# Kernel optimization log

Hardware: AMD Instinct MI355X
Metric: run time of the kernel (lower is better)

## Reference

```python
import jax, jax.numpy as jnp
import numpy as np

N = 50000      # total nodes
C = 128        # in_channels
G = 4          # num_groups
B = 50         # number of graphs
NPG = N // B   # nodes per graph = 1000
E = 250000     # total edges (intra-graph)
COUT = 128     # conv out_channels


def setup_inputs() -> dict:
    key = jax.random.key(0)
    ks = jax.random.split(key, 6)
    sc = 1.0 / np.sqrt(C)
    x = jax.random.normal(ks[0], (N, C), dtype=jnp.float32)
    W_group = jax.random.normal(ks[1], (C, G), dtype=jnp.float32) * sc
    W_self = jax.random.normal(ks[2], (C, COUT), dtype=jnp.float32) * sc
    W_nbr = jax.random.normal(ks[3], (C, COUT), dtype=jnp.float32) * sc
    b = jnp.zeros((COUT,), dtype=jnp.float32)
    # intra-graph edges: E//B edges per graph, endpoints offset by graph id
    epg = E // B
    offs = (jnp.arange(E, dtype=jnp.int32) // epg) * NPG
    src = offs + jax.random.randint(ks[4], (E,), 0, NPG, dtype=jnp.int32)
    dst = offs + jax.random.randint(ks[5], (E,), 0, NPG, dtype=jnp.int32)
    edge_index = jnp.stack([src, dst])
    batch = (jnp.arange(N, dtype=jnp.int32) // NPG)
    # expanded node e = i*G*NPG + g*NPG + j maps back to original node i*NPG + j
    eidx = jnp.arange(G * N, dtype=jnp.int32)
    group_ptr = (eidx // (G * NPG)) * NPG + (eidx % NPG)
    return dict(x=x, W_group=W_group, W_self=W_self, W_nbr=W_nbr, b=b,
                edge_index=edge_index, batch=batch, group_ptr=group_ptr)


def reference(x, W_group, W_self, W_nbr, b, edge_index, batch, group_ptr):
    # soft group assignment: s = softmax(x @ W_group).T -> [G, N]
    s = jax.nn.softmax(x @ W_group, axis=-1).T
    # outer-product expansion: [G, N, C]
    ex = s[:, :, None] * x[None, :, :]
    # per-graph cat ordering: (g, graph i, local j) -> i*G*NPG + g*NPG + j
    ex = ex.reshape(G, B, NPG, C).transpose(1, 0, 2, 3).reshape(G * N, C)
    # expanded adjacency: replicate each graph's edges once per group
    src, dst = edge_index[0], edge_index[1]
    goff = jnp.arange(G, dtype=src.dtype)[:, None] * NPG            # [G, 1]
    src_exp = ((src // NPG) * (G * NPG))[None, :] + goff + (src % NPG)[None, :]
    dst_exp = ((dst // NPG) * (G * NPG))[None, :] + goff + (dst % NPG)[None, :]
    src_exp = src_exp.reshape(-1)
    dst_exp = dst_exp.reshape(-1)
    # GraphConv on expanded graph: self transform + sum-aggregated neighbor transform
    msg = (ex @ W_nbr)[src_exp]                                      # [G*E, COUT]
    agg = jax.ops.segment_sum(msg, dst_exp, num_segments=G * N)
    out = ex @ W_self + agg + b                                      # [G*N, COUT]
    # scatter-reduce G group copies back onto N original nodes
    return jax.ops.segment_sum(out, group_ptr, num_segments=N)
```

## Files before the change

### kernel.cpp

```cpp
#include <hip/hip_runtime.h>

constexpr int N_NODES  = 50000;
constexpr int C_IN     = 128;
constexpr int C_OUT    = 128;
constexpr int E_EDGES  = 250000;
constexpr int G_GRP    = 4;
constexpr int NXCD     = 8;
constexpr int CAP      = 32;
constexpr int CAP1     = 8;
constexpr int TMF      = 64;


typedef __attribute__((ext_vector_type(8))) short     short8;
typedef __attribute__((ext_vector_type(4))) float     f32x4;
typedef __attribute__((ext_vector_type(2))) unsigned  u32x2;

__device__ __forceinline__ unsigned short f2bf(float f) {
    unsigned u = __builtin_bit_cast(unsigned, f);
    u += 0x7fffu + ((u >> 16) & 1u);
    return (unsigned short)(u >> 16);
}
__device__ __forceinline__ unsigned pack2(float lo, float hi) {
    return (unsigned)f2bf(lo) | ((unsigned)f2bf(hi) << 16);
}
__device__ __forceinline__ int xcd_swizzle(int bid, int nblocks) {
    int q = nblocks / NXCD, r = nblocks % NXCD;
    int xcd = bid % NXCD, lid = bid / NXCD;
    return (xcd < r ? xcd * (q + 1) : r * (q + 1) + (xcd - r) * q) + lid;
}

constexpr int BKT_I4   = N_NODES * CAP / 4;
constexpr int BKT_BLKS = (BKT_I4 + 255) / 256;
constexpr int CNT_BLKS = (N_NODES / 4 + 255) / 256;
constexpr int WT_BLKS  = (C_OUT * 256) / 256;

__global__ __launch_bounds__(256) void zero_prep_kernel(
    int* __restrict__ cnt, int* __restrict__ buckets,
    const float* __restrict__ Wself, const float* __restrict__ Wnbr,
    unsigned short* __restrict__ WT)
{
    int b = blockIdx.x;
    if (b < BKT_BLKS) {
        int idx = b * 256 + threadIdx.x;
        if (idx < BKT_I4) {
            int n = idx >> 3;
            reinterpret_cast<int4*>(buckets)[idx] = make_int4(n, n, n, n);
        }
    } else if (b < BKT_BLKS + CNT_BLKS) {
        int idx = (b - BKT_BLKS) * 256 + threadIdx.x;
        if (idx < N_NODES / 4)
            reinterpret_cast<int4*>(cnt)[idx] = make_int4(0, 0, 0, 0);
    } else {
        int idx = (b - BKT_BLKS - CNT_BLKS) * 256 + threadIdx.x;
        int c = idx >> 8, k = idx & 255;
        float v = (k < 128) ? Wself[k * C_OUT + c] : Wnbr[(k - 128) * C_OUT + c];
        WT[idx] = f2bf(v);
    }
}

constexpr int EDGE_BLOCKS = (E_EDGES + 255) / 256;

__global__ __launch_bounds__(256) void fill_kernel(
    const int* __restrict__ src, const int* __restrict__ dst,
    int* __restrict__ cnt, int* __restrict__ buckets)
{
    int e = blockIdx.x * 256 + threadIdx.x;
    if (e < E_EDGES) {
        int d = dst[e];
        int pos = atomicAdd(&cnt[d], 1);
        if (pos < CAP) buckets[(size_t)d * CAP + pos] = src[e];
    }
}

constexpr int FUSED_BLOCKS = (N_NODES + TMF - 1) / TMF;

__global__ __launch_bounds__(512, 2) void fused_kernel(
    const float* __restrict__ x,
    const int* __restrict__ cnt,
    const int* __restrict__ buckets,
    const unsigned short* __restrict__ WT,
    const float* __restrict__ bias,
    float* __restrict__ out)
{
    __shared__ unsigned char Ab[TMF * 512];

    int wg = xcd_swizzle(blockIdx.x, FUSED_BLOCKS);
    const int tid  = threadIdx.x;
    const int row0 = wg * TMF;

    #pragma unroll
    for (int i = 0; i < 4; ++i) {
        int idx = tid + i * 512;
        int r = idx >> 5, q = idx & 31;
        int n = row0 + r;
        float4 v = make_float4(0.f, 0.f, 0.f, 0.f);
        if (n < N_NODES) v = reinterpret_cast<const float4*>(x)[(size_t)n * 32 + q];
        int byte = (r * 512 + q * 8) ^ ((r & 7) << 4);
        *reinterpret_cast<u32x2*>(&Ab[byte]) = u32x2{pack2(v.x, v.y), pack2(v.z, v.w)};
    }

    {
        const int slot = tid >> 5;
        const int q    = tid & 31;
        const float4* x4 = reinterpret_cast<const float4*>(x);
        #pragma unroll
        for (int h = 0; h < 4; ++h) {
            int r  = slot + h * 16;
            int n  = row0 + r;
            int nc = (n < N_NODES) ? n : (N_NODES - 1);
            int d  = cnt[nc];
            if (d > CAP) d = CAP;
            if (n >= N_NODES) d = 0;
            const int4* sp4 = reinterpret_cast<const int4*>(buckets + (size_t)nc * CAP);

            float ax = 0.f, ay = 0.f, az = 0.f, aw = 0.f;
            {
                int4 sA = sp4[0], sB = sp4[1];
                int sl[8] = {sA.x, sA.y, sA.z, sA.w, sB.x, sB.y, sB.z, sB.w};
                #pragma unroll
                for (int k = 0; k < 8; ++k) {
                    float4 v = x4[(size_t)sl[k] * 32 + q];
                    if (k < d) { ax += v.x; ay += v.y; az += v.z; aw += v.w; }
                }
            }
            if (d > CAP1) {
                #pragma unroll
                for (int t = 0; t < 3; ++t) {
                    int4 sC = sp4[2 + 2 * t], sD = sp4[3 + 2 * t];
                    int sl[8] = {sC.x, sC.y, sC.z, sC.w, sD.x, sD.y, sD.z, sD.w};
                    #pragma unroll
                    for (int k = 0; k < 8; ++k) {
                        float4 v = x4[(size_t)sl[k] * 32 + q];
                        if (8 + t * 8 + k < d) { ax += v.x; ay += v.y; az += v.z; aw += v.w; }
                    }
                }
            }
            int byte = (r * 512 + 256 + q * 8) ^ ((r & 7) << 4);
            *reinterpret_cast<u32x2*>(&Ab[byte]) = u32x2{pack2(ax, ay), pack2(az, aw)};
        }
    }
    __syncthreads();

    const int lane = tid & 63;
    const int w    = tid >> 6;
    const int rt   = w >> 1;
    const int ct0  = (w & 1) * 4;

    short8 a[8];
    {
        int r  = rt * 16 + (lane & 15);
        int kb = (lane >> 4) * 16;
        #pragma unroll
        for (int ks = 0; ks < 8; ++ks) {
            int byte = (r * 512 + ks * 64 + kb) ^ ((r & 7) << 4);
            a[ks] = *reinterpret_cast<const short8*>(&Ab[byte]);
        }
    }

    #pragma unroll
    for (int cti = 0; cti < 4; ++cti) {
        int c = (ct0 + cti) * 16 + (lane & 15);
        const short8* bp = reinterpret_cast<const short8*>(WT + (size_t)c * 256)
                           + (lane >> 4);
        f32x4 acc = {0.f, 0.f, 0.f, 0.f};
        #pragma unroll
        for (int ks = 0; ks < 8; ++ks)
            acc = __builtin_amdgcn_mfma_f32_16x16x32_bf16(a[ks], bp[ks * 4],
                                                          acc, 0, 0, 0);
        float bv = (float)G_GRP * bias[c];
        #pragma unroll
        for (int ii = 0; ii < 4; ++ii) {
            int rr = row0 + rt * 16 + (lane >> 4) * 4 + ii;
            if (rr < N_NODES) out[(size_t)rr * C_OUT + c] = acc[ii] + bv;
        }
    }
}

extern "C" void kernel_launch(void* const* d_in, const int* in_sizes, int n_in,
                              void* d_out, int out_size, void* d_ws, size_t ws_size,
                              hipStream_t stream)
{
    const float* x     = (const float*)d_in[0];
    const float* Wself = (const float*)d_in[2];
    const float* Wnbr  = (const float*)d_in[3];
    const float* bias  = (const float*)d_in[4];
    const int*   eidx  = (const int*)d_in[5];

    const int* src = eidx;
    const int* dst = eidx + E_EDGES;

    int* cnt     = (int*)d_ws;
    int* buckets = cnt + N_NODES;
    unsigned short* WT = (unsigned short*)(buckets + (size_t)N_NODES * CAP);

    float* out = (float*)d_out;

    zero_prep_kernel<<<BKT_BLKS + CNT_BLKS + WT_BLKS, 256, 0, stream>>>(
        cnt, buckets, Wself, Wnbr, WT);

    fill_kernel<<<EDGE_BLOCKS, 256, 0, stream>>>(src, dst, cnt, buckets);

    fused_kernel<<<FUSED_BLOCKS, 512, 0, stream>>>(x, cnt, buckets, WT, bias, out);
}
```

Baseline: 70.25 us.

## Pre-convert x to bf16 for gathers and drop bucket pre-fill

A prep kernel now converts x to a bf16 copy once, and the fused kernel gathers neighbor rows from that copy, which halves the bytes per gather and skips per-use conversion. The bucket pre-fill (writing self indices) is removed; unused slots are masked by clamping their index to 0 and multiplying by a zero mask. The launch-bounds occupancy hint is dropped. This adds an extra full pass over x and sums neighbors from bf16-rounded inputs, which changes precision slightly.

Result: no change. 71.33 us (+1.5%).

```diff
diff --git a/kernel.cpp b/kernel.cpp
--- a/kernel.cpp
+++ b/kernel.cpp
@@ -14,6 +14,7 @@
 typedef __attribute__((ext_vector_type(8))) short     short8;
 typedef __attribute__((ext_vector_type(4))) float     f32x4;
 typedef __attribute__((ext_vector_type(2))) unsigned  u32x2;
+typedef __attribute__((ext_vector_type(4))) unsigned  u32x4;
 
 __device__ __forceinline__ unsigned short f2bf(float f) {
     unsigned u = __builtin_bit_cast(unsigned, f);
@@ -23,38 +24,45 @@
 __device__ __forceinline__ unsigned pack2(float lo, float hi) {
     return (unsigned)f2bf(lo) | ((unsigned)f2bf(hi) << 16);
 }
+__device__ __forceinline__ float bflo(unsigned u) {
+    return __builtin_bit_cast(float, u << 16);
+}
+__device__ __forceinline__ float bfhi(unsigned u) {
+    return __builtin_bit_cast(float, u & 0xffff0000u);
+}
 __device__ __forceinline__ int xcd_swizzle(int bid, int nblocks) {
     int q = nblocks / NXCD, r = nblocks % NXCD;
     int xcd = bid % NXCD, lid = bid / NXCD;
     return (xcd < r ? xcd * (q + 1) : r * (q + 1) + (xcd - r) * q) + lid;
 }
 
-constexpr int BKT_I4   = N_NODES * CAP / 4;
-constexpr int BKT_BLKS = (BKT_I4 + 255) / 256;
 constexpr int CNT_BLKS = (N_NODES / 4 + 255) / 256;
 constexpr int WT_BLKS  = (C_OUT * 256) / 256;
-
-__global__ __launch_bounds__(256) void zero_prep_kernel(
-    int* __restrict__ cnt, int* __restrict__ buckets,
+constexpr int XB_BLKS  = (N_NODES * 16) / 256;
+
+__global__ __launch_bounds__(256) void prep_kernel(
+    int* __restrict__ cnt,
     const float* __restrict__ Wself, const float* __restrict__ Wnbr,
-    unsigned short* __restrict__ WT)
+    unsigned short* __restrict__ WT,
+    const float* __restrict__ x, unsigned short* __restrict__ xb)
 {
     int b = blockIdx.x;
-    if (b < BKT_BLKS) {
+    if (b < CNT_BLKS) {
         int idx = b * 256 + threadIdx.x;
-        if (idx < BKT_I4) {
-            int n = idx >> 3;
-            reinterpret_cast<int4*>(buckets)[idx] = make_int4(n, n, n, n);
-        }
-    } else if (b < BKT_BLKS + CNT_BLKS) {
-        int idx = (b - BKT_BLKS) * 256 + threadIdx.x;
         if (idx < N_NODES / 4)
             reinterpret_cast<int4*>(cnt)[idx] = make_int4(0, 0, 0, 0);
-    } else {
-        int idx = (b - BKT_BLKS - CNT_BLKS) * 256 + threadIdx.x;
+    } else if (b < CNT_BLKS + WT_BLKS) {
+        int idx = (b - CNT_BLKS) * 256 + threadIdx.x;
         int c = idx >> 8, k = idx & 255;
         float v = (k < 128) ? Wself[k * C_OUT + c] : Wnbr[(k - 128) * C_OUT + c];
         WT[idx] = f2bf(v);
+    } else {
+        int idx = (b - CNT_BLKS - WT_BLKS) * 256 + threadIdx.x;
+        const float4* xp = reinterpret_cast<const float4*>(x) + (size_t)idx * 2;
+        float4 v0 = xp[0], v1 = xp[1];
+        u32x4 o{pack2(v0.x, v0.y), pack2(v0.z, v0.w),
+                pack2(v1.x, v1.y), pack2(v1.z, v1.w)};
+        reinterpret_cast<u32x4*>(xb)[idx] = o;
     }
 }
 
@@ -74,8 +82,8 @@
 
 constexpr int FUSED_BLOCKS = (N_NODES + TMF - 1) / TMF;
 
-__global__ __launch_bounds__(512, 2) void fused_kernel(
-    const float* __restrict__ x,
+__global__ __launch_bounds__(512) void fused_kernel(
+    const unsigned short* __restrict__ xb,
     const int* __restrict__ cnt,
     const int* __restrict__ buckets,
     const unsigned short* __restrict__ WT,
@@ -93,16 +101,17 @@
         int idx = tid + i * 512;
         int r = idx >> 5, q = idx & 31;
         int n = row0 + r;
-        float4 v = make_float4(0.f, 0.f, 0.f, 0.f);
-        if (n < N_NODES) v = reinterpret_cast<const float4*>(x)[(size_t)n * 32 + q];
+        u32x2 pk{0u, 0u};
+        if (n < N_NODES)
+            pk = *reinterpret_cast<const u32x2*>(&xb[(size_t)n * 128 + q * 4]);
         int byte = (r * 512 + q * 8) ^ ((r & 7) << 4);
-        *reinterpret_cast<u32x2*>(&Ab[byte]) = u32x2{pack2(v.x, v.y), pack2(v.z, v.w)};
+        *reinterpret_cast<u32x2*>(&Ab[byte]) = pk;
     }
 
     {
         const int slot = tid >> 5;
         const int q    = tid & 31;
-        const float4* x4 = reinterpret_cast<const float4*>(x);
+        const u32x2* xb2 = reinterpret_cast<const u32x2*>(xb);
         #pragma unroll
         for (int h = 0; h < 4; ++h) {
             int r  = slot + h * 16;
@@ -113,30 +122,57 @@
             if (n >= N_NODES) d = 0;
             const int4* sp4 = reinterpret_cast<const int4*>(buckets + (size_t)nc * CAP);
 
-            float ax = 0.f, ay = 0.f, az = 0.f, aw = 0.f;
+            float a0 = 0.f, a1 = 0.f, a2 = 0.f, a3 = 0.f;
             {
                 int4 sA = sp4[0], sB = sp4[1];
-                int sl[8] = {sA.x, sA.y, sA.z, sA.w, sB.x, sB.y, sB.z, sB.w};
-                #pragma unroll
-                for (int k = 0; k < 8; ++k) {
-                    float4 v = x4[(size_t)sl[k] * 32 + q];
-                    if (k < d) { ax += v.x; ay += v.y; az += v.z; aw += v.w; }
-                }
+                int s0 = (0 < d) ? sA.x : 0, s1 = (1 < d) ? sA.y : 0;
+                int s2 = (2 < d) ? sA.z : 0, s3 = (3 < d) ? sA.w : 0;
+                int s4 = (4 < d) ? sB.x : 0, s5 = (5 < d) ? sB.y : 0;
+                int s6 = (6 < d) ? sB.z : 0, s7 = (7 < d) ? sB.w : 0;
+                u32x2 w0 = xb2[(size_t)s0 * 32 + q];
+                u32x2 w1 = xb2[(size_t)s1 * 32 + q];
+                u32x2 w2 = xb2[(size_t)s2 * 32 + q];
+                u32x2 w3 = xb2[(size_t)s3 * 32 + q];
+                u32x2 w4 = xb2[(size_t)s4 * 32 + q];
+                u32x2 w5 = xb2[(size_t)s5 * 32 + q];
+                u32x2 w6 = xb2[(size_t)s6 * 32 + q];
+                u32x2 w7 = xb2[(size_t)s7 * 32 + q];
+                #define ACC(W, K)                                               \
+                    { float m = (K < d) ? 1.f : 0.f;                            \
+                      a0 = fmaf(m, bflo(W.x), a0); a1 = fmaf(m, bfhi(W.x), a1); \
+                      a2 = fmaf(m, bflo(W.y), a2); a3 = fmaf(m, bfhi(W.y), a3); }
+                ACC(w0, 0) ACC(w1, 1) ACC(w2, 2) ACC(w3, 3)
+                ACC(w4, 4) ACC(w5, 5) ACC(w6, 6) ACC(w7, 7)
             }
             if (d > CAP1) {
                 #pragma unroll
                 for (int t = 0; t < 3; ++t) {
                     int4 sC = sp4[2 + 2 * t], sD = sp4[3 + 2 * t];
-                    int sl[8] = {sC.x, sC.y, sC.z, sC.w, sD.x, sD.y, sD.z, sD.w};
-                    #pragma unroll
-                    for (int k = 0; k < 8; ++k) {
-                        float4 v = x4[(size_t)sl[k] * 32 + q];
-                        if (8 + t * 8 + k < d) { ax += v.x; ay += v.y; az += v.z; aw += v.w; }
-                    }
+                    int base = 8 + t * 8;
+                    int s0 = (base + 0 < d) ? sC.x : 0, s1 = (base + 1 < d) ? sC.y : 0;
+                    int s2 = (base + 2 < d) ? sC.z : 0, s3 = (base + 3 < d) ? sC.w : 0;
+                    int s4 = (base + 4 < d) ? sD.x : 0, s5 = (base + 5 < d) ? sD.y : 0;
+                    int s6 = (base + 6 < d) ? sD.z : 0, s7 = (base + 7 < d) ? sD.w : 0;
+                    u32x2 w0 = xb2[(size_t)s0 * 32 + q];
+                    u32x2 w1 = xb2[(size_t)s1 * 32 + q];
+                    u32x2 w2 = xb2[(size_t)s2 * 32 + q];
+                    u32x2 w3 = xb2[(size_t)s3 * 32 + q];
+                    u32x2 w4 = xb2[(size_t)s4 * 32 + q];
+                    u32x2 w5 = xb2[(size_t)s5 * 32 + q];
+                    u32x2 w6 = xb2[(size_t)s6 * 32 + q];
+                    u32x2 w7 = xb2[(size_t)s7 * 32 + q];
+                    #define ACC2(W, K)                                              \
+                        { float m = (base + K < d) ? 1.f : 0.f;                     \
+                          a0 = fmaf(m, bflo(W.x), a0); a1 = fmaf(m, bfhi(W.x), a1); \
+                          a2 = fmaf(m, bflo(W.y), a2); a3 = fmaf(m, bfhi(W.y), a3); }
+                    ACC2(w0, 0) ACC2(w1, 1) ACC2(w2, 2) ACC2(w3, 3)
+                    ACC2(w4, 4) ACC2(w5, 5) ACC2(w6, 6) ACC2(w7, 7)
+                    #undef ACC2
                 }
             }
+            #undef ACC
             int byte = (r * 512 + 256 + q * 8) ^ ((r & 7) << 4);
-            *reinterpret_cast<u32x2*>(&Ab[byte]) = u32x2{pack2(ax, ay), pack2(az, aw)};
+            *reinterpret_cast<u32x2*>(&Ab[byte]) = u32x2{pack2(a0, a1), pack2(a2, a3)};
         }
     }
     __syncthreads();
@@ -192,13 +228,14 @@
     int* cnt     = (int*)d_ws;
     int* buckets = cnt + N_NODES;
     unsigned short* WT = (unsigned short*)(buckets + (size_t)N_NODES * CAP);
+    unsigned short* xb = WT + (size_t)C_OUT * 256;
 
     float* out = (float*)d_out;
 
-    zero_prep_kernel<<<BKT_BLKS + CNT_BLKS + WT_BLKS, 256, 0, stream>>>(
-        cnt, buckets, Wself, Wnbr, WT);
+    prep_kernel<<<CNT_BLKS + WT_BLKS + XB_BLKS, 256, 0, stream>>>(
+        cnt, Wself, Wnbr, WT, x, xb);
 
     fill_kernel<<<EDGE_BLOCKS, 256, 0, stream>>>(src, dst, cnt, buckets);
 
-    fused_kernel<<<FUSED_BLOCKS, 512, 0, stream>>>(x, cnt, buckets, WT, bias, out);
-}
+    fused_kernel<<<FUSED_BLOCKS, 512, 0, stream>>>(xb, cnt, buckets, WT, bias, out);
+}
```

## Split neighbor gather into per-graph LDS-staged kernel feeding separate GEMM

Applied to the files above, without the earlier changes.

Moves the neighbor aggregation out of the fused GEMM into its own kernel. Each block stages one graph's 1000 nodes, for a 16-channel slice, as bf16 in shared memory and gathers neighbors from there instead of from global memory. The bucket pre-fill with self indices is dropped in favor of masked reads. The cost is an extra kernel launch and a bf16 round-trip of the aggregated features through global memory, and the kernel relies on edges staying within each graph.

After: 90.12 us. 28.3% more time.

```diff
diff --git a/kernel.cpp b/kernel.cpp
--- a/kernel.cpp
+++ b/kernel.cpp
@@ -5,9 +5,10 @@
 constexpr int C_OUT    = 128;
 constexpr int E_EDGES  = 250000;
 constexpr int G_GRP    = 4;
+constexpr int NPG      = 1000;
+constexpr int B_GRAPHS = 50;
 constexpr int NXCD     = 8;
 constexpr int CAP      = 32;
-constexpr int CAP1     = 8;
 constexpr int TMF      = 64;
 
 
@@ -23,35 +24,33 @@
 __device__ __forceinline__ unsigned pack2(float lo, float hi) {
     return (unsigned)f2bf(lo) | ((unsigned)f2bf(hi) << 16);
 }
+__device__ __forceinline__ float bflo(unsigned u) {
+    return __builtin_bit_cast(float, u << 16);
+}
+__device__ __forceinline__ float bfhi(unsigned u) {
+    return __builtin_bit_cast(float, u & 0xffff0000u);
+}
 __device__ __forceinline__ int xcd_swizzle(int bid, int nblocks) {
     int q = nblocks / NXCD, r = nblocks % NXCD;
     int xcd = bid % NXCD, lid = bid / NXCD;
     return (xcd < r ? xcd * (q + 1) : r * (q + 1) + (xcd - r) * q) + lid;
 }
 
-constexpr int BKT_I4   = N_NODES * CAP / 4;
-constexpr int BKT_BLKS = (BKT_I4 + 255) / 256;
 constexpr int CNT_BLKS = (N_NODES / 4 + 255) / 256;
 constexpr int WT_BLKS  = (C_OUT * 256) / 256;
 
-__global__ __launch_bounds__(256) void zero_prep_kernel(
-    int* __restrict__ cnt, int* __restrict__ buckets,
+__global__ __launch_bounds__(256) void k_prep(
+    int* __restrict__ cnt,
     const float* __restrict__ Wself, const float* __restrict__ Wnbr,
     unsigned short* __restrict__ WT)
 {
     int b = blockIdx.x;
-    if (b < BKT_BLKS) {
+    if (b < CNT_BLKS) {
         int idx = b * 256 + threadIdx.x;
-        if (idx < BKT_I4) {
-            int n = idx >> 3;
-            reinterpret_cast<int4*>(buckets)[idx] = make_int4(n, n, n, n);
-        }
-    } else if (b < BKT_BLKS + CNT_BLKS) {
-        int idx = (b - BKT_BLKS) * 256 + threadIdx.x;
         if (idx < N_NODES / 4)
             reinterpret_cast<int4*>(cnt)[idx] = make_int4(0, 0, 0, 0);
     } else {
-        int idx = (b - BKT_BLKS - CNT_BLKS) * 256 + threadIdx.x;
+        int idx = (b - CNT_BLKS) * 256 + threadIdx.x;
         int c = idx >> 8, k = idx & 255;
         float v = (k < 128) ? Wself[k * C_OUT + c] : Wnbr[(k - 128) * C_OUT + c];
         WT[idx] = f2bf(v);
@@ -60,7 +59,7 @@
 
 constexpr int EDGE_BLOCKS = (E_EDGES + 255) / 256;
 
-__global__ __launch_bounds__(256) void fill_kernel(
+__global__ __launch_bounds__(256) void k_fill(
     const int* __restrict__ src, const int* __restrict__ dst,
     int* __restrict__ cnt, int* __restrict__ buckets)
 {
@@ -72,19 +71,97 @@
     }
 }
 
-constexpr int FUSED_BLOCKS = (N_NODES + TMF - 1) / TMF;
-
-__global__ __launch_bounds__(512, 2) void fused_kernel(
+constexpr int GATHER_BLOCKS = B_GRAPHS * 8;
+
+__global__ __launch_bounds__(512, 1) void k_gather(
     const float* __restrict__ x,
     const int* __restrict__ cnt,
     const int* __restrict__ buckets,
+    unsigned short* __restrict__ xa_bf)
+{
+    __shared__ unsigned sxb[NPG * 8];
+
+    int b = xcd_swizzle(blockIdx.x, GATHER_BLOCKS);
+    const int tid = threadIdx.x;
+    const int g   = b >> 3;
+    const int oct = b & 7;
+    const int nb  = g * NPG;
+
+    {
+        const float4* x4 = reinterpret_cast<const float4*>(x);
+        for (int idx = tid; idx < NPG * 4; idx += 512) {
+            int r = idx >> 2, c4 = idx & 3;
+            float4 v = x4[(size_t)(nb + r) * 32 + oct * 4 + c4];
+            sxb[r * 8 + c4 * 2 + 0] = pack2(v.x, v.y);
+            sxb[r * 8 + c4 * 2 + 1] = pack2(v.z, v.w);
+        }
+    }
+    __syncthreads();
+
+    const int ln = tid & 7;
+    const int lg = tid >> 3;
+
+    for (int r = lg; r < NPG; r += 64) {
+        int n = nb + r;
+        int d = cnt[n];
+        if (d > CAP) d = CAP;
+        const int4* sp4 = reinterpret_cast<const int4*>(buckets + (size_t)n * CAP);
+
+        float a0 = 0.f, a1 = 0.f;
+        {
+            int4 sA = sp4[0], sB = sp4[1];
+            int t0 = ((0 < d) ? sA.x : nb) - nb, t1 = ((1 < d) ? sA.y : nb) - nb;
+            int t2 = ((2 < d) ? sA.z : nb) - nb, t3 = ((3 < d) ? sA.w : nb) - nb;
+            int t4 = ((4 < d) ? sB.x : nb) - nb, t5 = ((5 < d) ? sB.y : nb) - nb;
+            int t6 = ((6 < d) ? sB.z : nb) - nb, t7 = ((7 < d) ? sB.w : nb) - nb;
+            unsigned w0 = sxb[t0 * 8 + ln], w1 = sxb[t1 * 8 + ln];
+            unsigned w2 = sxb[t2 * 8 + ln], w3 = sxb[t3 * 8 + ln];
+            unsigned w4 = sxb[t4 * 8 + ln], w5 = sxb[t5 * 8 + ln];
+            unsigned w6 = sxb[t6 * 8 + ln], w7 = sxb[t7 * 8 + ln];
+            #define ACC(W, K)                                           \
+                { float m = (K < d) ? 1.f : 0.f;                        \
+                  a0 = fmaf(m, bflo(W), a0); a1 = fmaf(m, bfhi(W), a1); }
+            ACC(w0, 0) ACC(w1, 1) ACC(w2, 2) ACC(w3, 3)
+            ACC(w4, 4) ACC(w5, 5) ACC(w6, 6) ACC(w7, 7)
+            #undef ACC
+        }
+        if (d > 8) {
+            #pragma unroll
+            for (int t = 0; t < 3; ++t) {
+                int base = 8 + t * 8;
+                int4 sC = sp4[2 + 2 * t], sD = sp4[3 + 2 * t];
+                int t0 = ((base + 0 < d) ? sC.x : nb) - nb, t1 = ((base + 1 < d) ? sC.y : nb) - nb;
+                int t2 = ((base + 2 < d) ? sC.z : nb) - nb, t3 = ((base + 3 < d) ? sC.w : nb) - nb;
+                int t4 = ((base + 4 < d) ? sD.x : nb) - nb, t5 = ((base + 5 < d) ? sD.y : nb) - nb;
+                int t6 = ((base + 6 < d) ? sD.z : nb) - nb, t7 = ((base + 7 < d) ? sD.w : nb) - nb;
+                unsigned w0 = sxb[t0 * 8 + ln], w1 = sxb[t1 * 8 + ln];
+                unsigned w2 = sxb[t2 * 8 + ln], w3 = sxb[t3 * 8 + ln];
+                unsigned w4 = sxb[t4 * 8 + ln], w5 = sxb[t5 * 8 + ln];
+                unsigned w6 = sxb[t6 * 8 + ln], w7 = sxb[t7 * 8 + ln];
+                #define ACC2(W, K)                                          \
+                    { float m = (base + K < d) ? 1.f : 0.f;                 \
+                      a0 = fmaf(m, bflo(W), a0); a1 = fmaf(m, bfhi(W), a1); }
+                ACC2(w0, 0) ACC2(w1, 1) ACC2(w2, 2) ACC2(w3, 3)
+                ACC2(w4, 4) ACC2(w5, 5) ACC2(w6, 6) ACC2(w7, 7)
+                #undef ACC2
+            }
+        }
+        reinterpret_cast<unsigned*>(xa_bf)[(size_t)n * 64 + oct * 8 + ln] = pack2(a0, a1);
+    }
+}
+
+constexpr int GEMM_BLOCKS = (N_NODES + TMF - 1) / TMF;
+
+__global__ __launch_bounds__(512) void k_gemm(
+    const float* __restrict__ x,
+    const unsigned short* __restrict__ xa_bf,
     const unsigned short* __restrict__ WT,
     const float* __restrict__ bias,
     float* __restrict__ out)
 {
     __shared__ unsigned char Ab[TMF * 512];
 
-    int wg = xcd_swizzle(blockIdx.x, FUSED_BLOCKS);
+    int wg = xcd_swizzle(blockIdx.x, GEMM_BLOCKS);
     const int tid  = threadIdx.x;
     const int row0 = wg * TMF;
 
@@ -98,46 +175,16 @@
         int byte = (r * 512 + q * 8) ^ ((r & 7) << 4);
         *reinterpret_cast<u32x2*>(&Ab[byte]) = u32x2{pack2(v.x, v.y), pack2(v.z, v.w)};
     }
-
-    {
-        const int slot = tid >> 5;
-        const int q    = tid & 31;
-        const float4* x4 = reinterpret_cast<const float4*>(x);
-        #pragma unroll
-        for (int h = 0; h < 4; ++h) {
-            int r  = slot + h * 16;
-            int n  = row0 + r;
-            int nc = (n < N_NODES) ? n : (N_NODES - 1);
-            int d  = cnt[nc];
-            if (d > CAP) d = CAP;
-            if (n >= N_NODES) d = 0;
-            const int4* sp4 = reinterpret_cast<const int4*>(buckets + (size_t)nc * CAP);
-
-            float ax = 0.f, ay = 0.f, az = 0.f, aw = 0.f;
-            {
-                int4 sA = sp4[0], sB = sp4[1];
-                int sl[8] = {sA.x, sA.y, sA.z, sA.w, sB.x, sB.y, sB.z, sB.w};
-                #pragma unroll
-                for (int k = 0; k < 8; ++k) {
-                    float4 v = x4[(size_t)sl[k] * 32 + q];
-                    if (k < d) { ax += v.x; ay += v.y; az += v.z; aw += v.w; }
-                }
-            }
-            if (d > CAP1) {
-                #pragma unroll
-                for (int t = 0; t < 3; ++t) {
-                    int4 sC = sp4[2 + 2 * t], sD = sp4[3 + 2 * t];
-                    int sl[8] = {sC.x, sC.y, sC.z, sC.w, sD.x, sD.y, sD.z, sD.w};
-                    #pragma unroll
-                    for (int k = 0; k < 8; ++k) {
-                        float4 v = x4[(size_t)sl[k] * 32 + q];
-                        if (8 + t * 8 + k < d) { ax += v.x; ay += v.y; az += v.z; aw += v.w; }
-                    }
-                }
-            }
-            int byte = (r * 512 + 256 + q * 8) ^ ((r & 7) << 4);
-            *reinterpret_cast<u32x2*>(&Ab[byte]) = u32x2{pack2(ax, ay), pack2(az, aw)};
-        }
+    #pragma unroll
+    for (int i = 0; i < 4; ++i) {
+        int idx = tid + i * 512;
+        int r = idx >> 5, q = idx & 31;
+        int n = row0 + r;
+        u32x2 pk{0u, 0u};
+        if (n < N_NODES)
+            pk = *reinterpret_cast<const u32x2*>(&xa_bf[(size_t)n * 128 + q * 4]);
+        int byte = (r * 512 + 256 + q * 8) ^ ((r & 7) << 4);
+        *reinterpret_cast<u32x2*>(&Ab[byte]) = pk;
     }
     __syncthreads();
 
@@ -191,14 +238,16 @@
 
     int* cnt     = (int*)d_ws;
     int* buckets = cnt + N_NODES;
-    unsigned short* WT = (unsigned short*)(buckets + (size_t)N_NODES * CAP);
+    unsigned short* WT    = (unsigned short*)(buckets + (size_t)N_NODES * CAP);
+    unsigned short* xa_bf = WT + (size_t)C_OUT * 256;
 
     float* out = (float*)d_out;
 
-    zero_prep_kernel<<<BKT_BLKS + CNT_BLKS + WT_BLKS, 256, 0, stream>>>(
-        cnt, buckets, Wself, Wnbr, WT);
-
-    fill_kernel<<<EDGE_BLOCKS, 256, 0, stream>>>(src, dst, cnt, buckets);
-
-    fused_kernel<<<FUSED_BLOCKS, 512, 0, stream>>>(x, cnt, buckets, WT, bias, out);
-}
+    k_prep<<<CNT_BLKS + WT_BLKS, 256, 0, stream>>>(cnt, Wself, Wnbr, WT);
+
+    k_fill<<<EDGE_BLOCKS, 256, 0, stream>>>(src, dst, cnt, buckets);
+
+    k_gather<<<GATHER_BLOCKS, 512, 0, stream>>>(x, cnt, buckets, xa_bf);
+
+    k_gemm<<<GEMM_BLOCKS, 512, 0, stream>>>(x, xa_bf, WT, bias, out);
+}
```
